# Kernel tuning notes

Measured on AMD Instinct MI355X. Metric: run time of the kernel, lower is better.

## Reference

```python
import jax, jax.numpy as jnp
import numpy as np

BLOCK_SIZE = 3
SOBEL_PAD = 1  # sobel_size // 2
BLOCK_PAD = BLOCK_SIZE // 2

_SOBEL_X = jnp.array([[-1.0, 0.0, 1.0], [-2.0, 0.0, 2.0], [-1.0, 0.0, 1.0]], dtype=jnp.float32)[None, None]
_SOBEL_Y = jnp.array([[-1.0, -2.0, -1.0], [0.0, 0.0, 0.0], [1.0, 2.0, 1.0]], dtype=jnp.float32)[None, None]
_SUM_K = jnp.ones((1, 1, BLOCK_SIZE, BLOCK_SIZE), dtype=jnp.float32)


def _pad_replicate(x, p):
    return jnp.pad(x, ((0, 0), (0, 0), (p, p), (p, p)), mode='edge')


def _conv(x, k):
    return jax.lax.conv_general_dilated(
        x, k, window_strides=(1, 1), padding='VALID',
        dimension_numbers=('NCHW', 'OIHW', 'NCHW'))


def setup_inputs() -> dict:
    key = jax.random.key(0)
    image = jax.random.uniform(key, (8, 1, 1080, 1920), dtype=jnp.float32) * 255.0
    return {"image": image}


def reference(image) -> jnp.ndarray:
    img = image.astype(jnp.float32)
    img_p = _pad_replicate(img, SOBEL_PAD)
    Ix = _conv(img_p, _SOBEL_X)
    Iy = _conv(img_p, _SOBEL_Y)
    Ixx = Ix * Ix
    Iyy = Iy * Iy
    Ixy = Ix * Iy
    sum_Ixx = _conv(_pad_replicate(Ixx, BLOCK_PAD), _SUM_K)
    sum_Iyy = _conv(_pad_replicate(Iyy, BLOCK_PAD), _SUM_K)
    sum_Ixy = _conv(_pad_replicate(Ixy, BLOCK_PAD), _SUM_K)
    half_trace = (sum_Ixx + sum_Iyy) * 0.5
    diff_half = (sum_Ixx - sum_Iyy) * 0.5
    sqrt_disc = jnp.sqrt(diff_half * diff_half + sum_Ixy * sum_Ixy + 1e-10)
    lambda_min = half_trace - sqrt_disc
    return jnp.clip(lambda_min, 0.0)
```

## Files before the change

### kernel.cpp

```cpp
#include <hip/hip_runtime.h>

typedef float v2f __attribute__((ext_vector_type(2)));
typedef float v4f __attribute__((ext_vector_type(4)));

#define IMG_H 1080
#define IMG_W 1920
#define NBATCH 8
#define LSTRIP 9
#define BROWS (4*LSTRIP)
#define NK (LSTRIP+4)


static __device__ __forceinline__ v2f vfma2(v2f a, v2f b, v2f c) {
    return __builtin_elementwise_fma(a, b, c);
}
static __device__ __forceinline__ float bperm(int addr, float v) {
    return __int_as_float(__builtin_amdgcn_ds_bpermute(addr, __float_as_int(v)));
}

__global__ __launch_bounds__(256, 3)
void shi_tomasi_kernel(const float* __restrict__ img, float* __restrict__ out) {
    const int cg    = threadIdx.x & 63;
    const int strip = threadIdx.x >> 6;
    const int bx    = blockIdx.x;
    const int base  = bx * 240;
    const int cl    = min(max(base - 8 + 4 * cg, 0), IMG_W - 4);
    const int c0    = base + 4 * (cg - 2);
    const int s0    = blockIdx.y * BROWS + strip * LSTRIP;
    const float* g  = img + (size_t)blockIdx.z * (IMG_H * IMG_W);
    float* outb     = out + (size_t)blockIdx.z * (IMG_H * IMG_W);

    const bool eL     = (bx == 0) && (cg == 2);
    const bool eR     = (bx == 7) && (cg == 61);
    const bool doSt   = (cg >= 2) && (cg < 62);
    const int  aLft   = 4 * (cg - 1);
    const int  aRgt   = 4 * (cg + 1);
    const bool topFix = (s0 == 0);
    const bool botFix = (s0 + LSTRIP == IMG_H);

    v4f Zr[NK];
    const float* lp = g + cl;
    #pragma unroll
    for (int k = 0; k < NK; ++k) {
        int lr = s0 - 2 + k;
        lr = max(0, min(IMG_H - 1, lr));
        Zr[k] = *(const v4f*)(lp + (size_t)lr * IMG_W);
    }

    v2f hdR[3][3], hsR[3][3];
    float hfd[3], hfs[3];
    v2f hxx[3][2], hyy[3][2], hxy[3][2];
    const v2f two = {2.0f, 2.0f};

    #pragma unroll
    for (int k = 0; k < NK; ++k) {
        {
            const v4f Z = Zr[k];
            const float zl0 = bperm(aLft, Z.z), zl1 = bperm(aLft, Z.w);
            const float zr0 = bperm(aRgt, Z.x), zr1 = bperm(aRgt, Z.y);
            v2f Z0 = v2f{zl0, zl1};
            if (eL) Z0 = v2f{Z.x, Z.x};
            const v2f Z1 = v2f{Z.x, Z.y};
            const v2f Z2 = v2f{Z.z, Z.w};
            v2f Z3 = v2f{zr0, zr1};
            if (eR) Z3 = v2f{Z.w, Z.w};

            const v2f Sab = v2f{Z0.y, Z1.x};
            const v2f Sbc = v2f{Z1.y, Z2.x};
            const v2f Scd = v2f{Z2.y, Z3.x};
            v2f* hd = hdR[k % 3];
            v2f* hs = hsR[k % 3];
            hd[0] = Z1 - Z0; hd[1] = Z2 - Z1; hd[2] = Z3 - Z2;
            hs[0] = vfma2(Sab, two, Z0) + Z1;
            hs[1] = vfma2(Sbc, two, Z1) + Z2;
            hs[2] = vfma2(Scd, two, Z2) + Z3;
            hfd[k % 3] = eR ? (Z2.y - Z2.x) : (Z1.y - Z1.x);
            hfs[k % 3] = eR ? (Z2.x + 3.0f * Z2.y) : (3.0f * Z1.x + Z1.y);
        }

        if (k >= 2) {
            const int rr = k - 2;
            const int sm = rr % 3, sz = (rr + 1) % 3, sp = (rr + 2) % 3;

            v2f Ixp[3], Iyp[3];
            #pragma unroll
            for (int j = 0; j < 3; ++j) {
                Ixp[j] = vfma2(hdR[sz][j], two, hdR[sm][j]) + hdR[sp][j];
                Iyp[j] = hsR[sp][j] - hsR[sm][j];
            }
            const float ixf = hfd[sm] + 2.0f * hfd[sz] + hfd[sp];
            const float iyf = hfs[sp] - hfs[sm];
            if (eL) { Ixp[0].x = ixf; Iyp[0].x = iyf; }
            if (eR) { Ixp[2].y = ixf; Iyp[2].y = iyf; }

            v2f xx[3], yy[3], xy[3];
            #pragma unroll
            for (int j = 0; j < 3; ++j) {
                xx[j] = Ixp[j] * Ixp[j];
                yy[j] = Iyp[j] * Iyp[j];
                xy[j] = Ixp[j] * Iyp[j];
            }
            {
                v2f* hx = hxx[rr % 3];
                v2f* hy = hyy[rr % 3];
                v2f* hz = hxy[rr % 3];
                hx[0] = xx[0] + v2f{xx[0].y, xx[1].x} + xx[1];
                hx[1] = xx[1] + v2f{xx[1].y, xx[2].x} + xx[2];
                hy[0] = yy[0] + v2f{yy[0].y, yy[1].x} + yy[1];
                hy[1] = yy[1] + v2f{yy[1].y, yy[2].x} + yy[2];
                hz[0] = xy[0] + v2f{xy[0].y, xy[1].x} + xy[1];
                hz[1] = xy[1] + v2f{xy[1].y, xy[2].x} + xy[2];
            }
            if (rr == 1 && topFix) {
                #pragma unroll
                for (int q = 0; q < 2; ++q) {
                    hxx[0][q] = hxx[1][q]; hyy[0][q] = hyy[1][q]; hxy[0][q] = hxy[1][q];
                }
            }
            if (rr == LSTRIP + 1 && botFix) {
                #pragma unroll
                for (int q = 0; q < 2; ++q) {
                    hxx[rr % 3][q] = hxx[(rr - 1) % 3][q];
                    hyy[rr % 3][q] = hyy[(rr - 1) % 3][q];
                    hxy[rr % 3][q] = hxy[(rr - 1) % 3][q];
                }
            }

            if (rr >= 2) {
                const int a = (rr - 2) % 3, b2 = (rr - 1) % 3, c = rr % 3;
                float rv[4];
                #pragma unroll
                for (int q = 0; q < 2; ++q) {
                    const v2f sxx = hxx[a][q] + hxx[b2][q] + hxx[c][q];
                    const v2f syy = hyy[a][q] + hyy[b2][q] + hyy[c][q];
                    const v2f sxy = hxy[a][q] + hxy[b2][q] + hxy[c][q];
                    const v2f S = sxx + syy;
                    const v2f D = sxx - syy;
                    const v2f E = sxy + sxy;
                    const v2f disc = vfma2(D, D, vfma2(E, E, v2f{4e-10f, 4e-10f}));
                    const v2f qv = {__builtin_sqrtf(disc.x), __builtin_sqrtf(disc.y)};
                    const v2f lam = (S - qv) * 0.5f;
                    rv[2 * q]     = fmaxf(lam.x, 0.0f);
                    rv[2 * q + 1] = fmaxf(lam.y, 0.0f);
                }
                if (doSt) {
                    float* orowp = outb + (size_t)(s0 + rr - 2) * IMG_W + c0;
                    *(v4f*)orowp = v4f{rv[0], rv[1], rv[2], rv[3]};
                }
            }
        }
    }
}

extern "C" void kernel_launch(void* const* d_in, const int* in_sizes, int n_in,
                              void* d_out, int out_size, void* d_ws, size_t ws_size,
                              hipStream_t stream) {
    const float* img = (const float*)d_in[0];
    float* out = (float*)d_out;
    dim3 grid(8, IMG_H / BROWS, NBATCH);
    shi_tomasi_kernel<<<grid, 256, 0, stream>>>(img, out);
}
```

Baseline: 118.2 us.

## Replace full row preload with rolling prefetch ring and nontemporal stores

Instead of loading all 13 input rows into registers up front, the kernel keeps a 6-entry ring buffer and prefetches rows 4 ahead inside a two-iteration, non-unrolled loop built from a row-body macro. This is meant to cut register pressure and code size and to overlap loads with compute. Output stores also become nontemporal. The risk is less memory-level parallelism at startup and some control overhead from the runtime-predicated stages.

```diff
diff --git a/kernel.cpp b/kernel.cpp
--- a/kernel.cpp
+++ b/kernel.cpp
@@ -9,6 +9,8 @@
 #define LSTRIP 9
 #define BROWS (4*LSTRIP)
 #define NK (LSTRIP+4)
+#define PF 4
+#define ZS 6
 
 
 static __device__ __forceinline__ v2f vfma2(v2f a, v2f b, v2f c) {
@@ -38,12 +40,12 @@
     const bool topFix = (s0 == 0);
     const bool botFix = (s0 + LSTRIP == IMG_H);
 
-    v4f Zr[NK];
     const float* lp = g + cl;
+
+    v4f Zr[ZS];
     #pragma unroll
-    for (int k = 0; k < NK; ++k) {
-        int lr = s0 - 2 + k;
-        lr = max(0, min(IMG_H - 1, lr));
+    for (int k = 0; k < PF; ++k) {
+        int lr = max(0, min(IMG_H - 1, s0 - 2 + k));
         Zr[k] = *(const v4f*)(lp + (size_t)lr * IMG_W);
     }
 
@@ -52,104 +54,113 @@
     v2f hxx[3][2], hyy[3][2], hxy[3][2];
     const v2f two = {2.0f, 2.0f};
 
-    #pragma unroll
-    for (int k = 0; k < NK; ++k) {
-        {
-            const v4f Z = Zr[k];
-            const float zl0 = bperm(aLft, Z.z), zl1 = bperm(aLft, Z.w);
-            const float zr0 = bperm(aRgt, Z.x), zr1 = bperm(aRgt, Z.y);
-            v2f Z0 = v2f{zl0, zl1};
-            if (eL) Z0 = v2f{Z.x, Z.x};
-            const v2f Z1 = v2f{Z.x, Z.y};
-            const v2f Z2 = v2f{Z.z, Z.w};
-            v2f Z3 = v2f{zr0, zr1};
-            if (eR) Z3 = v2f{Z.w, Z.w};
+#define ROW_BODY(J, kk, doPre, doProd, doStore, doTFix, doBFix) do {         \
+    constexpr int ZP = (J) % ZS, ZQ = ((J) + PF) % ZS;                       \
+    constexpr int P0 = (J) % 3, P1 = ((J) + 1) % 3, P2 = ((J) + 2) % 3;      \
+    if (doPre) {                                                             \
+        int lr = min(IMG_H - 1, s0 + (kk) + 2);              \
+        Zr[ZQ] = *(const v4f*)(lp + (size_t)lr * IMG_W);                     \
+    }                                                                        \
+    {                                                                        \
+        const v4f Z = Zr[ZP];                                                \
+        const float zl0 = bperm(aLft, Z.z), zl1 = bperm(aLft, Z.w);          \
+        const float zr0 = bperm(aRgt, Z.x), zr1 = bperm(aRgt, Z.y);          \
+        v2f Z0 = v2f{zl0, zl1};                                              \
+        if (eL) Z0 = v2f{Z.x, Z.x};                     \
+        const v2f Z1 = v2f{Z.x, Z.y};                                        \
+        const v2f Z2 = v2f{Z.z, Z.w};                                        \
+        v2f Z3 = v2f{zr0, zr1};                                              \
+        if (eR) Z3 = v2f{Z.w, Z.w};                   \
+        const v2f Sab = v2f{Z0.y, Z1.x};                                     \
+        const v2f Sbc = v2f{Z1.y, Z2.x};                                     \
+        const v2f Scd = v2f{Z2.y, Z3.x};                                     \
+        hdR[P0][0] = Z1 - Z0; hdR[P0][1] = Z2 - Z1; hdR[P0][2] = Z3 - Z2;    \
+        hsR[P0][0] = vfma2(Sab, two, Z0) + Z1;                               \
+        hsR[P0][1] = vfma2(Sbc, two, Z1) + Z2;                               \
+        hsR[P0][2] = vfma2(Scd, two, Z2) + Z3;                               \
+        hfd[P0] = eR ? (Z2.y - Z2.x) : (Z1.y - Z1.x);                        \
+        hfs[P0] = eR ? (Z2.x + 3.0f * Z2.y) : (3.0f * Z1.x + Z1.y);          \
+    }                                                                        \
+    if (doProd) {                                                            \
+        v2f Ixp[3], Iyp[3];                                                  \
+        _Pragma("unroll")                                                    \
+        for (int j = 0; j < 3; ++j) {                                        \
+            Ixp[j] = vfma2(hdR[P2][j], two, hdR[P1][j]) + hdR[P0][j];        \
+            Iyp[j] = hsR[P0][j] - hsR[P1][j];                                \
+        }                                                                    \
+        const float ixf = hfd[P1] + 2.0f * hfd[P2] + hfd[P0];                \
+        const float iyf = hfs[P0] - hfs[P1];                                 \
+        if (eL) { Ixp[0].x = ixf; Iyp[0].x = iyf; }                          \
+        if (eR) { Ixp[2].y = ixf; Iyp[2].y = iyf; }                          \
+        v2f xx[3], yy[3], xy[3];                                             \
+        _Pragma("unroll")                                                    \
+        for (int j = 0; j < 3; ++j) {                                        \
+            xx[j] = Ixp[j] * Ixp[j];                                         \
+            yy[j] = Iyp[j] * Iyp[j];                                         \
+            xy[j] = Ixp[j] * Iyp[j];                                         \
+        }                                                                    \
+        hxx[P1][0] = xx[0] + v2f{xx[0].y, xx[1].x} + xx[1];                  \
+        hxx[P1][1] = xx[1] + v2f{xx[1].y, xx[2].x} + xx[2];                  \
+        hyy[P1][0] = yy[0] + v2f{yy[0].y, yy[1].x} + yy[1];                  \
+        hyy[P1][1] = yy[1] + v2f{yy[1].y, yy[2].x} + yy[2];                  \
+        hxy[P1][0] = xy[0] + v2f{xy[0].y, xy[1].x} + xy[1];                  \
+        hxy[P1][1] = xy[1] + v2f{xy[1].y, xy[2].x} + xy[2];                  \
+        if ((doTFix) && topFix) {                         \
+            _Pragma("unroll")                                                \
+            for (int q = 0; q < 2; ++q) {                                    \
+                hxx[P0][q] = hxx[P1][q];                                     \
+                hyy[P0][q] = hyy[P1][q];                                     \
+                hxy[P0][q] = hxy[P1][q];                                     \
+            }                                                                \
+        }                                                                    \
+        if ((doBFix) && botFix) {                        \
+            _Pragma("unroll")                                                \
+            for (int q = 0; q < 2; ++q) {                                    \
+                hxx[P1][q] = hxx[P0][q];                                     \
+                hyy[P1][q] = hyy[P0][q];                                     \
+                hxy[P1][q] = hxy[P0][q];                                     \
+            }                                                                \
+        }                                                                    \
+        if (doStore) {                                                       \
+            float rv[4];                                                     \
+            _Pragma("unroll")                                                \
+            for (int q = 0; q < 2; ++q) {                                    \
+                const v2f sxx = hxx[P2][q] + hxx[P0][q] + hxx[P1][q];        \
+                const v2f syy = hyy[P2][q] + hyy[P0][q] + hyy[P1][q];        \
+                const v2f sxy = hxy[P2][q] + hxy[P0][q] + hxy[P1][q];        \
+                const v2f S = sxx + syy;                                     \
+                const v2f D = sxx - syy;                                     \
+                const v2f E = sxy + sxy;                                     \
+                const v2f disc = vfma2(D, D, vfma2(E, E, v2f{4e-10f, 4e-10f})); \
+                const v2f qv = {__builtin_sqrtf(disc.x), __builtin_sqrtf(disc.y)}; \
+                const v2f lam = (S - qv) * 0.5f;                             \
+                rv[2 * q]     = fmaxf(lam.x, 0.0f);                          \
+                rv[2 * q + 1] = fmaxf(lam.y, 0.0f);                          \
+            }                                                                \
+            if (doSt) {                                                      \
+                float* orowp = outb + (size_t)(s0 + (kk) - 4) * IMG_W + c0;  \
+                __builtin_nontemporal_store(v4f{rv[0], rv[1], rv[2], rv[3]}, \
+                                            (v4f*)orowp);                    \
+            }                                                                \
+        }                                                                    \
+    }                                                                        \
+} while (0)
 
-            const v2f Sab = v2f{Z0.y, Z1.x};
-            const v2f Sbc = v2f{Z1.y, Z2.x};
-            const v2f Scd = v2f{Z2.y, Z3.x};
-            v2f* hd = hdR[k % 3];
-            v2f* hs = hsR[k % 3];
-            hd[0] = Z1 - Z0; hd[1] = Z2 - Z1; hd[2] = Z3 - Z2;
-            hs[0] = vfma2(Sab, two, Z0) + Z1;
-            hs[1] = vfma2(Sbc, two, Z1) + Z2;
-            hs[2] = vfma2(Scd, two, Z2) + Z3;
-            hfd[k % 3] = eR ? (Z2.y - Z2.x) : (Z1.y - Z1.x);
-            hfs[k % 3] = eR ? (Z2.x + 3.0f * Z2.y) : (3.0f * Z1.x + Z1.y);
-        }
+    int k = 0;
+    #pragma clang loop unroll(disable)
+    for (int it = 0; it < 2; ++it) {
+        const bool w = (it != 0);
+        const bool f = (it == 0);
+        ROW_BODY(0, k, true,  w,    w,    false, false); ++k;
+        ROW_BODY(1, k, true,  w,    w,    false, false); ++k;
+        ROW_BODY(2, k, true,  true, w,    false, false); ++k;
+        ROW_BODY(3, k, f,     true, w,    f,     false); ++k;
+        ROW_BODY(4, k, f,     true, true, false, false); ++k;
+        ROW_BODY(5, k, f,     true, true, false, false); ++k;
+    }
+    ROW_BODY(0, k, false, true, true, false, true);
 
-        if (k >= 2) {
-            const int rr = k - 2;
-            const int sm = rr % 3, sz = (rr + 1) % 3, sp = (rr + 2) % 3;
-
-            v2f Ixp[3], Iyp[3];
-            #pragma unroll
-            for (int j = 0; j < 3; ++j) {
-                Ixp[j] = vfma2(hdR[sz][j], two, hdR[sm][j]) + hdR[sp][j];
-                Iyp[j] = hsR[sp][j] - hsR[sm][j];
-            }
-            const float ixf = hfd[sm] + 2.0f * hfd[sz] + hfd[sp];
-            const float iyf = hfs[sp] - hfs[sm];
-            if (eL) { Ixp[0].x = ixf; Iyp[0].x = iyf; }
-            if (eR) { Ixp[2].y = ixf; Iyp[2].y = iyf; }
-
-            v2f xx[3], yy[3], xy[3];
-            #pragma unroll
-            for (int j = 0; j < 3; ++j) {
-                xx[j] = Ixp[j] * Ixp[j];
-                yy[j] = Iyp[j] * Iyp[j];
-                xy[j] = Ixp[j] * Iyp[j];
-            }
-            {
-                v2f* hx = hxx[rr % 3];
-                v2f* hy = hyy[rr % 3];
-                v2f* hz = hxy[rr % 3];
-                hx[0] = xx[0] + v2f{xx[0].y, xx[1].x} + xx[1];
-                hx[1] = xx[1] + v2f{xx[1].y, xx[2].x} + xx[2];
-                hy[0] = yy[0] + v2f{yy[0].y, yy[1].x} + yy[1];
-                hy[1] = yy[1] + v2f{yy[1].y, yy[2].x} + yy[2];
-                hz[0] = xy[0] + v2f{xy[0].y, xy[1].x} + xy[1];
-                hz[1] = xy[1] + v2f{xy[1].y, xy[2].x} + xy[2];
-            }
-            if (rr == 1 && topFix) {
-                #pragma unroll
-                for (int q = 0; q < 2; ++q) {
-                    hxx[0][q] = hxx[1][q]; hyy[0][q] = hyy[1][q]; hxy[0][q] = hxy[1][q];
-                }
-            }
-            if (rr == LSTRIP + 1 && botFix) {
-                #pragma unroll
-                for (int q = 0; q < 2; ++q) {
-                    hxx[rr % 3][q] = hxx[(rr - 1) % 3][q];
-                    hyy[rr % 3][q] = hyy[(rr - 1) % 3][q];
-                    hxy[rr % 3][q] = hxy[(rr - 1) % 3][q];
-                }
-            }
-
-            if (rr >= 2) {
-                const int a = (rr - 2) % 3, b2 = (rr - 1) % 3, c = rr % 3;
-                float rv[4];
-                #pragma unroll
-                for (int q = 0; q < 2; ++q) {
-                    const v2f sxx = hxx[a][q] + hxx[b2][q] + hxx[c][q];
-                    const v2f syy = hyy[a][q] + hyy[b2][q] + hyy[c][q];
-                    const v2f sxy = hxy[a][q] + hxy[b2][q] + hxy[c][q];
-                    const v2f S = sxx + syy;
-                    const v2f D = sxx - syy;
-                    const v2f E = sxy + sxy;
-                    const v2f disc = vfma2(D, D, vfma2(E, E, v2f{4e-10f, 4e-10f}));
-                    const v2f qv = {__builtin_sqrtf(disc.x), __builtin_sqrtf(disc.y)};
-                    const v2f lam = (S - qv) * 0.5f;
-                    rv[2 * q]     = fmaxf(lam.x, 0.0f);
-                    rv[2 * q + 1] = fmaxf(lam.y, 0.0f);
-                }
-                if (doSt) {
-                    float* orowp = outb + (size_t)(s0 + rr - 2) * IMG_W + c0;
-                    *(v4f*)orowp = v4f{rv[0], rv[1], rv[2], rv[3]};
-                }
-            }
-        }
-    }
+#undef ROW_BODY
 }
 
 extern "C" void kernel_launch(void* const* d_in, const int* in_sizes, int n_in,
```

Result: no change. 117.6 us (-0.4%).
